# Performance work log

Hardware: AMD Instinct MI355X
Metric: run time of the kernel (lower is better)

Reference implementation:

```python
import jax, jax.numpy as jnp
import numpy as np

NUM_HEADS = 8
D_MODEL = 256
D_K = 256
SEQ = 32
FFT_HEAD = 3  # heads >= 3 operate in the FFT domain and are IFFT'd after
NEG = jnp.float32(1e10)


def _fft_t(x):
    # x: (..., 32, 256) real. Interleaved real/imag pairs -> complex 2D FFT over (4,2).
    lead = x.shape[:-2]
    xr = x.reshape(lead + (16, 32, 4, 2, 2))
    xc = jax.lax.complex(xr[..., 0], xr[..., 1])      # (..., 16, 32, 4, 2)
    y = jnp.fft.fft2(xc)                              # over last two axes
    out = jnp.concatenate([jnp.real(y), jnp.imag(y)], axis=-1)  # (...,16,32,4,4)
    return out.reshape(lead + (SEQ, D_MODEL))


def _ifft_t(x):
    lead = x.shape[:-2]
    xr = x.reshape(lead + (16, 32, 4, 2, 2))
    xc = jax.lax.complex(xr[..., 0], xr[..., 1])
    y = jnp.fft.ifft2(xc)
    out = jnp.concatenate([jnp.real(y), jnp.imag(y)], axis=-1)
    return out.reshape(lead + (SEQ, D_MODEL))


def _atrous_mask():
    i = jnp.arange(SEQ)[:, None]
    j = jnp.arange(SEQ)[None, :]
    return (jnp.abs(i - j) % 2 == 0).astype(jnp.float32)  # (32, 32)


def _attn_group(x, Wq_g, Wk_g, Wv_g, mask):
    # x: (B, S, D); W*_g: (H, D, K); mask: (S, S)
    Q = jnp.einsum('bsd,hdk->bhsk', x, Wq_g)
    K = jnp.einsum('bsd,hdk->bhsk', x, Wk_g)
    V = jnp.einsum('bsd,hdk->bhsk', x, Wv_g)
    scores = jnp.einsum('bhsk,bhtk->bhst', Q, K) / jnp.sqrt(jnp.float32(D_K))
    scores = scores * mask - NEG * (1.0 - mask)
    A = jax.nn.softmax(scores, axis=-1)
    return jnp.einsum('bhst,bhtk->bhsk', A, V)  # (B, H, S, K)


def setup_inputs() -> dict:
    key = jax.random.key(0)
    k0, k1, k2, k3 = jax.random.split(key, 4)
    B = 4096
    glorot = float(np.sqrt(2.0 / (D_MODEL + D_K)))
    return {
        'inputs': jax.random.normal(k0, (B, 1, SEQ, D_MODEL), dtype=jnp.float32),
        'Wq': jax.random.normal(k1, (NUM_HEADS, D_MODEL, D_K), dtype=jnp.float32) * glorot,
        'Wk': jax.random.normal(k2, (NUM_HEADS, D_MODEL, D_K), dtype=jnp.float32) * glorot,
        'Wv': jax.random.normal(k3, (NUM_HEADS, D_MODEL, D_K), dtype=jnp.float32) * glorot,
    }


def reference(inputs, Wq, Wk, Wv):
    # inputs: (B, 1, 32, 256)
    x = inputs[:, 0]                                  # (B, 32, 256)
    mask = _atrous_mask()
    # Heads 0..2: plain domain
    out_lo = _attn_group(x, Wq[:FFT_HEAD], Wk[:FFT_HEAD], Wv[:FFT_HEAD], mask)
    # Heads 3..: FFT domain, outputs IFFT'd per head
    xf = _fft_t(x)
    out_hi = _attn_group(xf, Wq[FFT_HEAD:], Wk[FFT_HEAD:], Wv[FFT_HEAD:], mask)
    out_hi = _ifft_t(out_hi)
    total = out_lo.sum(axis=1) + out_hi.sum(axis=1)   # (B, 32, 256)
    return (total / NUM_HEADS)[:, None]               # (B, 1, 32, 256)
```

## Files before the change

### kernel.cpp

```cpp
#include <hip/hip_runtime.h>

typedef _Float16 f16;
typedef _Float16 f16x4 __attribute__((ext_vector_type(4)));
typedef _Float16 f16x8 __attribute__((ext_vector_type(8)));
typedef float    f32x4 __attribute__((ext_vector_type(4)));

#define MFMA_F16(a,b,c) __builtin_amdgcn_mfma_f32_16x16x32_f16((a),(b),(c),0,0,0)

__device__ __forceinline__ float T_val(int rr, int cc) {
  int p = rr >> 2, f = rr & 3;
  int c = cc >> 2, d = (cc >> 1) & 1, e = cc & 1;
  int q = f & 1;
  int m = (p * c + 2 * q * d) & 3;
  float cs = (m == 0) ? 1.f : (m == 2) ? -1.f : 0.f;
  float sn = (m == 1) ? 1.f : (m == 3) ? -1.f : 0.f;
  if (f < 2) return (e == 0) ? cs : sn;
  return (e == 0) ? -sn : cs;
}
__device__ __forceinline__ float U_val(int rr, int cc) {
  int p = rr >> 2, f = rr & 3;
  int c = cc >> 2, d = (cc >> 1) & 1, e = cc & 1;
  int q = f & 1;
  int m = (p * c + 2 * q * d) & 3;
  float cs = (m == 0) ? 1.f : (m == 2) ? -1.f : 0.f;
  float sn = (m == 1) ? 1.f : (m == 3) ? -1.f : 0.f;
  float v;
  if (f < 2) v = (e == 0) ? cs : -sn;
  else       v = (e == 0) ? sn : cs;
  return v * 0.125f;
}

__global__ void prep_qk(const float* __restrict__ Wq, const float* __restrict__ Wk,
                        float* __restrict__ WqE, float* __restrict__ WkE) {
  int b = blockIdx.x;
  int isK = b >> 11;
  int h = (b >> 8) & 7;
  int dd = b & 255;
  const float* W = isK ? Wk : Wq;
  float* E = isK ? WkE : WqE;
  int k = threadIdx.x;
  size_t base = (size_t)h * 65536;
  float v;
  if (h < 3) {
    v = W[base + (size_t)dd * 256 + k];
  } else {
    int g = dd >> 4, i = dd & 15;
    float s = 0.f;
    for (int ip = 0; ip < 16; ++ip) {
      float t = T_val(ip, i);
      if (t != 0.f) s += t * W[base + (size_t)(g * 16 + ip) * 256 + k];
    }
    v = s;
  }
  E[base + (size_t)dd * 256 + k] = v;
}

__global__ void prep_m(const float* __restrict__ WqE, const float* __restrict__ WkE,
                       f16* __restrict__ Mt) {
  __shared__ float Aq[32][33];
  __shared__ float Bk[32][33];
  int h = blockIdx.x >> 6;
  int dpt = (blockIdx.x >> 3) & 7;
  int dt = blockIdx.x & 7;
  int tid = threadIdx.x;
  int drow = tid & 31;
  int dprow4 = (tid >> 5) * 4;
  float acc0 = 0.f, acc1 = 0.f, acc2 = 0.f, acc3 = 0.f;
  int r = tid >> 3;
  int c0 = (tid & 7) * 4;
  for (int kt = 0; kt < 8; ++kt) {
    for (int j = 0; j < 4; ++j) {
      Aq[r][c0 + j] = WqE[(size_t)h * 65536 + (size_t)(dt * 32 + r) * 256 + kt * 32 + c0 + j];
      Bk[r][c0 + j] = WkE[(size_t)h * 65536 + (size_t)(dpt * 32 + r) * 256 + kt * 32 + c0 + j];
    }
    __syncthreads();
    #pragma unroll
    for (int k = 0; k < 32; ++k) {
      float a = Aq[drow][k];
      acc0 += a * Bk[dprow4 + 0][k];
      acc1 += a * Bk[dprow4 + 1][k];
      acc2 += a * Bk[dprow4 + 2][k];
      acc3 += a * Bk[dprow4 + 3][k];
    }
    __syncthreads();
  }
  int d_ = dt * 32 + drow;
  size_t ob = (size_t)h * 65536 + (size_t)(dpt * 32 + dprow4) * 256 + d_;
  Mt[ob + 0 * 256] = (f16)(acc0 * 0.0625f);
  Mt[ob + 1 * 256] = (f16)(acc1 * 0.0625f);
  Mt[ob + 2 * 256] = (f16)(acc2 * 0.0625f);
  Mt[ob + 3 * 256] = (f16)(acc3 * 0.0625f);
}

__global__ void prep_v(const float* __restrict__ Wv, f16* __restrict__ Wvt) {
  __shared__ float Ts[16][16];
  __shared__ float Us[16][16];
  int h = blockIdx.x >> 8;
  int kp = blockIdx.x & 255;
  int tid = threadIdx.x;
  Ts[tid >> 4][tid & 15] = T_val(tid >> 4, tid & 15);
  Us[tid >> 4][tid & 15] = U_val(tid >> 4, tid & 15);
  __syncthreads();
  int d = tid;
  int g = d >> 4, i = d & 15;
  int gp = kp >> 4, fp = kp & 15;
  float s = 0.f;
  if (h < 3) {
    s = Wv[(size_t)h * 65536 + (size_t)d * 256 + kp];
  } else {
    for (int ip = 0; ip < 16; ++ip) {
      float tv = Ts[ip][i];
      if (tv != 0.f) {
        float inner = 0.f;
        for (int j = 0; j < 16; ++j) {
          float uv = Us[fp][j];
          if (uv != 0.f)
            inner += uv * Wv[(size_t)h * 65536 + (size_t)(g * 16 + ip) * 256 + gp * 16 + j];
        }
        s += tv * inner;
      }
    }
  }
  Wvt[(size_t)h * 65536 + (size_t)kp * 256 + d] = (f16)(s * 0.125f);
}

__device__ __forceinline__ int swz(int row, int col) { return col ^ ((row & 7) << 3); }

__global__ __launch_bounds__(512, 2) void mha_main(
    const float* __restrict__ xg_all,
    const f16* __restrict__ MtG,
    const f16* __restrict__ WvtG,
    float* __restrict__ outG)
{
  extern __shared__ char smem[];
  f16* Xs  = (f16*)smem;
  f16* Y   = (f16*)(smem + 65536);
  f16* VT  = (f16*)(smem + 65536);
  f16* Aat = (f16*)(smem + 135168);

  const int tid = threadIdx.x;
  const int w   = tid >> 6;
  const int l   = tid & 63;
  const int l15 = l & 15;
  const int l4  = l >> 4;

  f32x4 acc[8][2];
  #pragma unroll
  for (int i = 0; i < 8; ++i) {
    acc[i][0] = (f32x4){0.f, 0.f, 0.f, 0.f};
    acc[i][1] = (f32x4){0.f, 0.f, 0.f, 0.f};
  }

  const float* xg = xg_all + (size_t)blockIdx.x * 32768;
  #pragma unroll
  for (int i = 0; i < 16; ++i) {
    int f4 = i * 512 + tid;
    int row = f4 >> 6;
    int col = (f4 & 63) << 2;
    f32x4 v = *(const f32x4*)(xg + (size_t)f4 * 4);
    f16x4 hv = __builtin_convertvector(v, f16x4);
    *(f16x4*)(Xs + row * 256 + swz(row, col)) = hv;
  }
  __syncthreads();

  for (int h = 0; h < 8; ++h) {
    const f16* MtH = MtG + (size_t)h * 65536;
    const f16* WvH = WvtG + (size_t)h * 65536;

    f32x4 C0[8], C1[8];
    #pragma unroll
    for (int nt = 0; nt < 8; ++nt) {
      C0[nt] = (f32x4){0.f, 0.f, 0.f, 0.f};
      C1[nt] = (f32x4){0.f, 0.f, 0.f, 0.f};
    }
    {
      int arow = w * 32 + l15;
      #pragma unroll
      for (int kt = 0; kt < 8; ++kt) {
        int ks = kt * 32 + l4 * 8;
        f16x8 a0 = *(const f16x8*)(MtH + (size_t)arow * 256 + ks);
        f16x8 a1 = *(const f16x8*)(MtH + (size_t)(arow + 16) * 256 + ks);
        #pragma unroll
        for (int nt = 0; nt < 8; ++nt) {
          int xrow = nt * 16 + l15;
          f16x8 b = *(const f16x8*)(Xs + xrow * 256 + swz(xrow, ks));
          C0[nt] = MFMA_F16(a0, b, C0[nt]);
          C1[nt] = MFMA_F16(a1, b, C1[nt]);
        }
      }
      #pragma unroll
      for (int nt = 0; nt < 8; ++nt) {
        int srow = nt * 16 + l15;
        int dc0 = w * 32 + l4 * 4;
        *(f16x4*)(Y + srow * 256 + swz(srow, dc0)) = __builtin_convertvector(C0[nt], f16x4);
        *(f16x4*)(Y + srow * 256 + swz(srow, dc0 + 16)) = __builtin_convertvector(C1[nt], f16x4);
      }
    }
    __syncthreads();

    {
      int bq = w >> 1, mt = w & 1;
      f32x4 S0 = (f32x4){0.f, 0.f, 0.f, 0.f};
      f32x4 S1 = (f32x4){0.f, 0.f, 0.f, 0.f};
      int yrow = bq * 32 + mt * 16 + l15;
      int x0 = bq * 32 + l15;
      int x1 = bq * 32 + 16 + l15;
      #pragma unroll
      for (int kt = 0; kt < 8; ++kt) {
        int ks = kt * 32 + l4 * 8;
        f16x8 ay = *(const f16x8*)(Y + yrow * 256 + swz(yrow, ks));
        f16x8 b0 = *(const f16x8*)(Xs + x0 * 256 + swz(x0, ks));
        f16x8 b1 = *(const f16x8*)(Xs + x1 * 256 + swz(x1, ks));
        S0 = MFMA_F16(ay, b0, S0);
        S1 = MFMA_F16(ay, b1, S1);
      }
      #pragma unroll
      for (int r = 0; r < 4; ++r) {
        bool valid = ((l & 1) == (r & 1));
        float v0 = valid ? S0[r] : -1e30f;
        float v1 = valid ? S1[r] : -1e30f;
        float mx = fmaxf(v0, v1);
        mx = fmaxf(mx, __shfl_xor(mx, 1));
        mx = fmaxf(mx, __shfl_xor(mx, 2));
        mx = fmaxf(mx, __shfl_xor(mx, 4));
        mx = fmaxf(mx, __shfl_xor(mx, 8));
        float e0 = valid ? __expf(v0 - mx) : 0.f;
        float e1 = valid ? __expf(v1 - mx) : 0.f;
        float sm = e0 + e1;
        sm += __shfl_xor(sm, 1);
        sm += __shfl_xor(sm, 2);
        sm += __shfl_xor(sm, 4);
        sm += __shfl_xor(sm, 8);
        float inv = 1.f / sm;
        int s = mt * 16 + l4 * 4 + r;
        Aat[(bq * 32 + s) * 40 + l15] = (f16)(e0 * inv);
        Aat[(bq * 32 + s) * 40 + 16 + l15] = (f16)(e1 * inv);
      }
    }
    __syncthreads();

    f32x4 Cv0[8], Cv1[8];
    #pragma unroll
    for (int mt = 0; mt < 8; ++mt) {
      Cv0[mt] = (f32x4){0.f, 0.f, 0.f, 0.f};
      Cv1[mt] = (f32x4){0.f, 0.f, 0.f, 0.f};
    }
    {
      int bcol = w * 32 + l15;
      #pragma unroll
      for (int kt = 0; kt < 8; ++kt) {
        int ks = kt * 32 + l4 * 8;
        f16x8 b0 = *(const f16x8*)(WvH + (size_t)bcol * 256 + ks);
        f16x8 b1 = *(const f16x8*)(WvH + (size_t)(bcol + 16) * 256 + ks);
        #pragma unroll
        for (int mt = 0; mt < 8; ++mt) {
          int xrow = mt * 16 + l15;
          f16x8 a = *(const f16x8*)(Xs + xrow * 256 + swz(xrow, ks));
          Cv0[mt] = MFMA_F16(a, b0, Cv0[mt]);
          Cv1[mt] = MFMA_F16(a, b1, Cv1[mt]);
        }
      }
      #pragma unroll
      for (int mt = 0; mt < 8; ++mt) {
        int sp = mt * 16 + l4 * 4;
        int kp0 = w * 32 + l15;
        *(f16x4*)(VT + kp0 * 136 + sp) = __builtin_convertvector(Cv0[mt], f16x4);
        *(f16x4*)(VT + (kp0 + 16) * 136 + sp) = __builtin_convertvector(Cv1[mt], f16x4);
      }
    }
    __syncthreads();

    {
      int bo = w >> 1, kh = w & 1;
      f16x8 bf0 = *(const f16x8*)(Aat + (bo * 32 + l15) * 40 + l4 * 8);
      f16x8 bf1 = *(const f16x8*)(Aat + (bo * 32 + 16 + l15) * 40 + l4 * 8);
      #pragma unroll
      for (int mt = 0; mt < 8; ++mt) {
        int kp = kh * 128 + mt * 16 + l15;
        f16x8 av = *(const f16x8*)(VT + kp * 136 + bo * 32 + l4 * 8);
        acc[mt][0] = MFMA_F16(av, bf0, acc[mt][0]);
        acc[mt][1] = MFMA_F16(av, bf1, acc[mt][1]);
      }
    }
    __syncthreads();
  }

  {
    int bo = w >> 1, kh = w & 1;
    float* outB = outG + ((size_t)blockIdx.x * 4 + bo) * 8192;
    #pragma unroll
    for (int mt = 0; mt < 8; ++mt) {
      #pragma unroll
      for (int nt = 0; nt < 2; ++nt) {
        int s = nt * 16 + l15;
        int kp = kh * 128 + mt * 16 + l4 * 4;
        *(f32x4*)(outB + s * 256 + kp) = acc[mt][nt];
      }
    }
  }
}

extern "C" void kernel_launch(void* const* d_in, const int* in_sizes, int n_in,
                              void* d_out, int out_size, void* d_ws, size_t ws_size,
                              hipStream_t stream) {
  const float* x  = (const float*)d_in[0];
  const float* Wq = (const float*)d_in[1];
  const float* Wk = (const float*)d_in[2];
  const float* Wv = (const float*)d_in[3];
  float* out = (float*)d_out;
  char* ws = (char*)d_ws;
  float* WqE = (float*)ws;
  float* WkE = (float*)(ws + 2097152);
  f16*   Mt  = (f16*)(ws + 4194304);
  f16*   Wvt = (f16*)(ws + 5242880);

  prep_qk<<<4096, 256, 0, stream>>>(Wq, Wk, WqE, WkE);
  prep_m<<<512, 256, 0, stream>>>(WqE, WkE, Mt);
  prep_v<<<2048, 256, 0, stream>>>(Wv, Wvt);
  mha_main<<<1024, 512, 145408, stream>>>(x, Mt, Wvt, out);
}
```

Baseline: 437.3 us.

## Restructure attention kernel around 32x32 MFMA with register-resident intermediates

The main kernel now handles 8 batch elements per block (half as many blocks) and switches from 16x16x32 to 32x32x16 MFMAs. Each wave processes two batches and one head per pass. The Y (x·M) and V projections stay in registers and feed the score and output MFMAs directly, so the Y and V^T round-trips through LDS go away. Only the softmax probabilities go through shared memory, with two syncs per head pair instead of four per head. The costs are heavier register pressure, larger LDS use per block, and fewer blocks to fill the GPU.

Result: slower. 724.0 us (+65.6%).

```diff
diff --git a/kernel.cpp b/kernel.cpp
--- a/kernel.cpp
+++ b/kernel.cpp
@@ -4,8 +4,9 @@
 typedef _Float16 f16x4 __attribute__((ext_vector_type(4)));
 typedef _Float16 f16x8 __attribute__((ext_vector_type(8)));
 typedef float    f32x4 __attribute__((ext_vector_type(4)));
-
-#define MFMA_F16(a,b,c) __builtin_amdgcn_mfma_f32_16x16x32_f16((a),(b),(c),0,0,0)
+typedef float    f32x16 __attribute__((ext_vector_type(16)));
+
+#define MFMA32(a,b,c) __builtin_amdgcn_mfma_f32_32x32x16_f16((a),(b),(c),0,0,0)
 
 __device__ __forceinline__ float T_val(int rr, int cc) {
   int p = rr >> 2, f = rr & 3;
@@ -69,9 +70,9 @@
   int r = tid >> 3;
   int c0 = (tid & 7) * 4;
   for (int kt = 0; kt < 8; ++kt) {
-    for (int j = 0; j < 4; ++j) {
-      Aq[r][c0 + j] = WqE[(size_t)h * 65536 + (size_t)(dt * 32 + r) * 256 + kt * 32 + c0 + j];
-      Bk[r][c0 + j] = WkE[(size_t)h * 65536 + (size_t)(dpt * 32 + r) * 256 + kt * 32 + c0 + j];
+    for (int jj = 0; jj < 4; ++jj) {
+      Aq[r][c0 + jj] = WqE[(size_t)h * 65536 + (size_t)(dt * 32 + r) * 256 + kt * 32 + c0 + jj];
+      Bk[r][c0 + jj] = WkE[(size_t)h * 65536 + (size_t)(dpt * 32 + r) * 256 + kt * 32 + c0 + jj];
     }
     __syncthreads();
     #pragma unroll
@@ -112,10 +113,10 @@
       float tv = Ts[ip][i];
       if (tv != 0.f) {
         float inner = 0.f;
-        for (int j = 0; j < 16; ++j) {
-          float uv = Us[fp][j];
+        for (int jj = 0; jj < 16; ++jj) {
+          float uv = Us[fp][jj];
           if (uv != 0.f)
-            inner += uv * Wv[(size_t)h * 65536 + (size_t)(g * 16 + ip) * 256 + gp * 16 + j];
+            inner += uv * Wv[(size_t)h * 65536 + (size_t)(g * 16 + ip) * 256 + gp * 16 + jj];
         }
         s += tv * inner;
       }
@@ -124,7 +125,51 @@
   Wvt[(size_t)h * 65536 + (size_t)kp * 256 + d] = (f16)(s * 0.125f);
 }
 
-__device__ __forceinline__ int swz(int row, int col) { return col ^ ((row & 7) << 3); }
+__device__ __forceinline__ f16x8 cvt_lo(const f32x16& c) {
+  f16x8 r;
+  #pragma unroll
+  for (int i = 0; i < 8; ++i) r[i] = (f16)c[i];
+  return r;
+}
+__device__ __forceinline__ f16x8 cvt_hi(const f32x16& c) {
+  f16x8 r;
+  #pragma unroll
+  for (int i = 0; i < 8; ++i) r[i] = (f16)c[8 + i];
+  return r;
+}
+__device__ __forceinline__ f16x8 comb(f16x4 a, f16x4 b) {
+  f16x8 r;
+  #pragma unroll
+  for (int i = 0; i < 4; ++i) { r[i] = a[i]; r[4 + i] = b[i]; }
+  return r;
+}
+
+__device__ __forceinline__ void softmax_store(const f32x16& S, f16* Pb, int s, int H) {
+  int s1 = s & 1;
+  float mx = -1e30f;
+  #pragma unroll
+  for (int rr = 0; rr < 16; ++rr) {
+    float v = ((rr & 1) == s1) ? S[rr] : -1e30f;
+    mx = fmaxf(mx, v);
+  }
+  mx = fmaxf(mx, __shfl_xor(mx, 32));
+  float e[16];
+  float sum = 0.f;
+  #pragma unroll
+  for (int rr = 0; rr < 16; ++rr) {
+    float v = ((rr & 1) == s1) ? __expf(S[rr] - mx) : 0.f;
+    e[rr] = v;
+    sum += v;
+  }
+  sum += __shfl_xor(sum, 32);
+  float inv = 1.f / sum;
+  int px = (s & 7) << 2;
+  #pragma unroll
+  for (int rr = 0; rr < 16; ++rr) {
+    int t = (rr & 3) + 8 * (rr >> 2) + 4 * H;
+    Pb[s * 32 + (t ^ px)] = (f16)(e[rr] * inv);
+  }
+}
 
 __global__ __launch_bounds__(512, 2) void mha_main(
     const float* __restrict__ xg_all,
@@ -133,168 +178,130 @@
     float* __restrict__ outG)
 {
   extern __shared__ char smem[];
-  f16* Xs  = (f16*)smem;
-  f16* Y   = (f16*)(smem + 65536);
-  f16* VT  = (f16*)(smem + 65536);
-  f16* Aat = (f16*)(smem + 135168);
+  f16* Xs = (f16*)smem;
+  f16* Pl = (f16*)(smem + 131072);
 
   const int tid = threadIdx.x;
   const int w   = tid >> 6;
-  const int l   = tid & 63;
-  const int l15 = l & 15;
-  const int l4  = l >> 4;
-
-  f32x4 acc[8][2];
-  #pragma unroll
-  for (int i = 0; i < 8; ++i) {
-    acc[i][0] = (f32x4){0.f, 0.f, 0.f, 0.f};
-    acc[i][1] = (f32x4){0.f, 0.f, 0.f, 0.f};
-  }
-
-  const float* xg = xg_all + (size_t)blockIdx.x * 32768;
-  #pragma unroll
-  for (int i = 0; i < 16; ++i) {
+  const int l31 = tid & 31;
+  const int H   = (tid >> 5) & 1;
+  const int bp  = w >> 1;
+  const int j   = w & 1;
+
+  const float* xg = xg_all + (size_t)blockIdx.x * 65536;
+  #pragma unroll 4
+  for (int i = 0; i < 32; ++i) {
     int f4 = i * 512 + tid;
     int row = f4 >> 6;
-    int col = (f4 & 63) << 2;
+    int col4 = (f4 & 63) << 2;
     f32x4 v = *(const f32x4*)(xg + (size_t)f4 * 4);
-    f16x4 hv = __builtin_convertvector(v, f16x4);
-    *(f16x4*)(Xs + row * 256 + swz(row, col)) = hv;
+    f16x4 hv;
+    hv[0] = (f16)v[0]; hv[1] = (f16)v[1]; hv[2] = (f16)v[2]; hv[3] = (f16)v[3];
+    *(f16x4*)(Xs + row * 256 + (col4 ^ ((row & 7) << 3))) = hv;
   }
   __syncthreads();
 
-  for (int h = 0; h < 8; ++h) {
-    const f16* MtH = MtG + (size_t)h * 65536;
-    const f16* WvH = WvtG + (size_t)h * 65536;
-
-    f32x4 C0[8], C1[8];
+  const int b0 = bp * 2, b1 = b0 + 1;
+  const f16* Xr0 = Xs + (b0 * 32 + l31) * 256;
+  const f16* Xr1 = Xs + (b1 * 32 + l31) * 256;
+  const int rx = (l31 & 7) << 3;
+
+  f32x16 acc[2][4];
+  #pragma unroll
+  for (int bb = 0; bb < 2; ++bb)
     #pragma unroll
-    for (int nt = 0; nt < 8; ++nt) {
-      C0[nt] = (f32x4){0.f, 0.f, 0.f, 0.f};
-      C1[nt] = (f32x4){0.f, 0.f, 0.f, 0.f};
-    }
+    for (int t4 = 0; t4 < 4; ++t4)
+      #pragma unroll
+      for (int i = 0; i < 16; ++i) acc[bb][t4][i] = 0.f;
+
+  for (int r = 0; r < 4; ++r) {
     {
-      int arow = w * 32 + l15;
+      const f16* MtH = MtG + (size_t)(2 * r + j) * 65536;
+      f32x16 S0, S1;
       #pragma unroll
-      for (int kt = 0; kt < 8; ++kt) {
-        int ks = kt * 32 + l4 * 8;
-        f16x8 a0 = *(const f16x8*)(MtH + (size_t)arow * 256 + ks);
-        f16x8 a1 = *(const f16x8*)(MtH + (size_t)(arow + 16) * 256 + ks);
+      for (int i = 0; i < 16; ++i) { S0[i] = 0.f; S1[i] = 0.f; }
+      for (int dt = 0; dt < 8; ++dt) {
+        f32x16 Y0, Y1;
         #pragma unroll
-        for (int nt = 0; nt < 8; ++nt) {
-          int xrow = nt * 16 + l15;
-          f16x8 b = *(const f16x8*)(Xs + xrow * 256 + swz(xrow, ks));
-          C0[nt] = MFMA_F16(a0, b, C0[nt]);
-          C1[nt] = MFMA_F16(a1, b, C1[nt]);
+        for (int i = 0; i < 16; ++i) { Y0[i] = 0.f; Y1[i] = 0.f; }
+        const f16* Arow = MtH + (size_t)(dt * 32 + l31) * 256 + H * 8;
+        #pragma unroll 4
+        for (int kt = 0; kt < 16; ++kt) {
+          f16x8 a = *(const f16x8*)(Arow + kt * 16);
+          int sc = (kt * 16 + H * 8) ^ rx;
+          f16x8 xb0 = *(const f16x8*)(Xr0 + sc);
+          f16x8 xb1 = *(const f16x8*)(Xr1 + sc);
+          Y0 = MFMA32(a, xb0, Y0);
+          Y1 = MFMA32(a, xb1, Y1);
         }
+        int c0 = (dt * 32 + 4 * H) ^ rx;
+        int c1 = (dt * 32 + 4 * H + 8) ^ rx;
+        int c2 = (dt * 32 + 16 + 4 * H) ^ rx;
+        int c3 = (dt * 32 + 24 + 4 * H) ^ rx;
+        f16x8 alo0 = comb(*(const f16x4*)(Xr0 + c0), *(const f16x4*)(Xr0 + c1));
+        f16x8 ahi0 = comb(*(const f16x4*)(Xr0 + c2), *(const f16x4*)(Xr0 + c3));
+        f16x8 alo1 = comb(*(const f16x4*)(Xr1 + c0), *(const f16x4*)(Xr1 + c1));
+        f16x8 ahi1 = comb(*(const f16x4*)(Xr1 + c2), *(const f16x4*)(Xr1 + c3));
+        S0 = MFMA32(alo0, cvt_lo(Y0), S0);
+        S0 = MFMA32(ahi0, cvt_hi(Y0), S0);
+        S1 = MFMA32(alo1, cvt_lo(Y1), S1);
+        S1 = MFMA32(ahi1, cvt_hi(Y1), S1);
       }
+      softmax_store(S0, Pl + (j * 8 + b0) * 1024, l31, H);
+      softmax_store(S1, Pl + (j * 8 + b1) * 1024, l31, H);
+    }
+    __syncthreads();
+    #pragma unroll
+    for (int hh = 0; hh < 2; ++hh) {
+      const f16* WvH = WvtG + (size_t)(2 * r + hh) * 65536;
+      const f16* Pb0 = Pl + (hh * 8 + b0) * 1024 + l31 * 32;
+      const f16* Pb1 = Pl + (hh * 8 + b1) * 1024 + l31 * 32;
+      int px = (l31 & 7) << 2;
+      f16x8 P0lo = comb(*(const f16x4*)(Pb0 + ((4 * H) ^ px)),
+                        *(const f16x4*)(Pb0 + ((4 * H + 8) ^ px)));
+      f16x8 P0hi = comb(*(const f16x4*)(Pb0 + ((16 + 4 * H) ^ px)),
+                        *(const f16x4*)(Pb0 + ((24 + 4 * H) ^ px)));
+      f16x8 P1lo = comb(*(const f16x4*)(Pb1 + ((4 * H) ^ px)),
+                        *(const f16x4*)(Pb1 + ((4 * H + 8) ^ px)));
+      f16x8 P1hi = comb(*(const f16x4*)(Pb1 + ((16 + 4 * H) ^ px)),
+                        *(const f16x4*)(Pb1 + ((24 + 4 * H) ^ px)));
       #pragma unroll
-      for (int nt = 0; nt < 8; ++nt) {
-        int srow = nt * 16 + l15;
-        int dc0 = w * 32 + l4 * 4;
-        *(f16x4*)(Y + srow * 256 + swz(srow, dc0)) = __builtin_convertvector(C0[nt], f16x4);
-        *(f16x4*)(Y + srow * 256 + swz(srow, dc0 + 16)) = __builtin_convertvector(C1[nt], f16x4);
+      for (int t4 = 0; t4 < 4; ++t4) {
+        const f16* Wrow = WvH + (size_t)((j * 4 + t4) * 32 + l31) * 256 + H * 8;
+        f32x16 V0, V1;
+        #pragma unroll
+        for (int i = 0; i < 16; ++i) { V0[i] = 0.f; V1[i] = 0.f; }
+        #pragma unroll 4
+        for (int kt = 0; kt < 16; ++kt) {
+          f16x8 wv = *(const f16x8*)(Wrow + kt * 16);
+          int sc = (kt * 16 + H * 8) ^ rx;
+          f16x8 xa0 = *(const f16x8*)(Xr0 + sc);
+          f16x8 xa1 = *(const f16x8*)(Xr1 + sc);
+          V0 = MFMA32(xa0, wv, V0);
+          V1 = MFMA32(xa1, wv, V1);
+        }
+        acc[0][t4] = MFMA32(cvt_lo(V0), P0lo, acc[0][t4]);
+        acc[0][t4] = MFMA32(cvt_hi(V0), P0hi, acc[0][t4]);
+        acc[1][t4] = MFMA32(cvt_lo(V1), P1lo, acc[1][t4]);
+        acc[1][t4] = MFMA32(cvt_hi(V1), P1hi, acc[1][t4]);
       }
     }
     __syncthreads();
-
-    {
-      int bq = w >> 1, mt = w & 1;
-      f32x4 S0 = (f32x4){0.f, 0.f, 0.f, 0.f};
-      f32x4 S1 = (f32x4){0.f, 0.f, 0.f, 0.f};
-      int yrow = bq * 32 + mt * 16 + l15;
-      int x0 = bq * 32 + l15;
-      int x1 = bq * 32 + 16 + l15;
+  }
+
+  #pragma unroll
+  for (int bb = 0; bb < 2; ++bb) {
+    float* ob = outG + ((size_t)blockIdx.x * 8 + (bp * 2 + bb)) * 8192 + l31 * 256 + j * 128;
+    #pragma unroll
+    for (int t4 = 0; t4 < 4; ++t4) {
       #pragma unroll
-      for (int kt = 0; kt < 8; ++kt) {
-        int ks = kt * 32 + l4 * 8;
-        f16x8 ay = *(const f16x8*)(Y + yrow * 256 + swz(yrow, ks));
-        f16x8 b0 = *(const f16x8*)(Xs + x0 * 256 + swz(x0, ks));
-        f16x8 b1 = *(const f16x8*)(Xs + x1 * 256 + swz(x1, ks));
-        S0 = MFMA_F16(ay, b0, S0);
-        S1 = MFMA_F16(ay, b1, S1);
-      }
-      #pragma unroll
-      for (int r = 0; r < 4; ++r) {
-        bool valid = ((l & 1) == (r & 1));
-        float v0 = valid ? S0[r] : -1e30f;
-        float v1 = valid ? S1[r] : -1e30f;
-        float mx = fmaxf(v0, v1);
-        mx = fmaxf(mx, __shfl_xor(mx, 1));
-        mx = fmaxf(mx, __shfl_xor(mx, 2));
-        mx = fmaxf(mx, __shfl_xor(mx, 4));
-        mx = fmaxf(mx, __shfl_xor(mx, 8));
-        float e0 = valid ? __expf(v0 - mx) : 0.f;
-        float e1 = valid ? __expf(v1 - mx) : 0.f;
-        float sm = e0 + e1;
-        sm += __shfl_xor(sm, 1);
-        sm += __shfl_xor(sm, 2);
-        sm += __shfl_xor(sm, 4);
-        sm += __shfl_xor(sm, 8);
-        float inv = 1.f / sm;
-        int s = mt * 16 + l4 * 4 + r;
-        Aat[(bq * 32 + s) * 40 + l15] = (f16)(e0 * inv);
-        Aat[(bq * 32 + s) * 40 + 16 + l15] = (f16)(e1 * inv);
-      }
-    }
-    __syncthreads();
-
-    f32x4 Cv0[8], Cv1[8];
-    #pragma unroll
-    for (int mt = 0; mt < 8; ++mt) {
-      Cv0[mt] = (f32x4){0.f, 0.f, 0.f, 0.f};
-      Cv1[mt] = (f32x4){0.f, 0.f, 0.f, 0.f};
-    }
-    {
-      int bcol = w * 32 + l15;
-      #pragma unroll
-      for (int kt = 0; kt < 8; ++kt) {
-        int ks = kt * 32 + l4 * 8;
-        f16x8 b0 = *(const f16x8*)(WvH + (size_t)bcol * 256 + ks);
-        f16x8 b1 = *(const f16x8*)(WvH + (size_t)(bcol + 16) * 256 + ks);
-        #pragma unroll
-        for (int mt = 0; mt < 8; ++mt) {
-          int xrow = mt * 16 + l15;
-          f16x8 a = *(const f16x8*)(Xs + xrow * 256 + swz(xrow, ks));
-          Cv0[mt] = MFMA_F16(a, b0, Cv0[mt]);
-          Cv1[mt] = MFMA_F16(a, b1, Cv1[mt]);
-        }
-      }
-      #pragma unroll
-      for (int mt = 0; mt < 8; ++mt) {
-        int sp = mt * 16 + l4 * 4;
-        int kp0 = w * 32 + l15;
-        *(f16x4*)(VT + kp0 * 136 + sp) = __builtin_convertvector(Cv0[mt], f16x4);
-        *(f16x4*)(VT + (kp0 + 16) * 136 + sp) = __builtin_convertvector(Cv1[mt], f16x4);
-      }
-    }
-    __syncthreads();
-
-    {
-      int bo = w >> 1, kh = w & 1;
-      f16x8 bf0 = *(const f16x8*)(Aat + (bo * 32 + l15) * 40 + l4 * 8);
-      f16x8 bf1 = *(const f16x8*)(Aat + (bo * 32 + 16 + l15) * 40 + l4 * 8);
-      #pragma unroll
-      for (int mt = 0; mt < 8; ++mt) {
-        int kp = kh * 128 + mt * 16 + l15;
-        f16x8 av = *(const f16x8*)(VT + kp * 136 + bo * 32 + l4 * 8);
-        acc[mt][0] = MFMA_F16(av, bf0, acc[mt][0]);
-        acc[mt][1] = MFMA_F16(av, bf1, acc[mt][1]);
-      }
-    }
-    __syncthreads();
-  }
-
-  {
-    int bo = w >> 1, kh = w & 1;
-    float* outB = outG + ((size_t)blockIdx.x * 4 + bo) * 8192;
-    #pragma unroll
-    for (int mt = 0; mt < 8; ++mt) {
-      #pragma unroll
-      for (int nt = 0; nt < 2; ++nt) {
-        int s = nt * 16 + l15;
-        int kp = kh * 128 + mt * 16 + l4 * 4;
-        *(f32x4*)(outB + s * 256 + kp) = acc[mt][nt];
+      for (int q = 0; q < 4; ++q) {
+        f32x4 v;
+        v[0] = acc[bb][t4][q * 4 + 0];
+        v[1] = acc[bb][t4][q * 4 + 1];
+        v[2] = acc[bb][t4][q * 4 + 2];
+        v[3] = acc[bb][t4][q * 4 + 3];
+        *(f32x4*)(ob + t4 * 32 + q * 8 + H * 4) = v;
       }
     }
   }
@@ -317,5 +324,5 @@
   prep_qk<<<4096, 256, 0, stream>>>(Wq, Wk, WqE, WkE);
   prep_m<<<512, 256, 0, stream>>>(WqE, WkE, Mt);
   prep_v<<<2048, 256, 0, stream>>>(Wv, Wvt);
-  mha_main<<<1024, 512, 145408, stream>>>(x, Mt, Wvt, out);
-}
+  mha_main<<<512, 512, 163840, stream>>>(x, Mt, Wvt, out);
+}
```

## Keep V in registers, retile per-head GEMMs, and pre-pack weights into MFMA fragment layout

Applied to the files above, without the earlier changes.

Weights Mt and Wvt are repacked by a new small kernel into a layout ordered by MFMA fragment, so each lane loads its operand with one coalesced 16-byte read. The per-head Q·M and X·Wv GEMMs are retiled into 4x4 and 2x2x4 register blocks per wave, which raises operand reuse. The V projection result now stays in registers as packed f16 and feeds the A·V MFMA directly. This removes the VT shared-memory staging and one barrier per head, in exchange for higher register pressure and an extra launch.

New measurement: 430.6 us. Within noise of the previous version (-1.5%).

```diff
diff --git a/kernel.cpp b/kernel.cpp
--- a/kernel.cpp
+++ b/kernel.cpp
@@ -4,8 +4,21 @@
 typedef _Float16 f16x4 __attribute__((ext_vector_type(4)));
 typedef _Float16 f16x8 __attribute__((ext_vector_type(8)));
 typedef float    f32x4 __attribute__((ext_vector_type(4)));
+typedef unsigned int u32;
 
 #define MFMA_F16(a,b,c) __builtin_amdgcn_mfma_f32_16x16x32_f16((a),(b),(c),0,0,0)
+
+__device__ __forceinline__ u32 pkf16(float a, float b) {
+  return __builtin_bit_cast(u32, __builtin_amdgcn_cvt_pkrtz(a, b));
+}
+union F8U4 { u32 d[4]; f16x8 v; };
+
+__device__ __forceinline__ f16x8 comb(f16x4 a, f16x4 b) {
+  f16x8 r;
+  #pragma unroll
+  for (int i = 0; i < 4; ++i) { r[i] = a[i]; r[4 + i] = b[i]; }
+  return r;
+}
 
 __device__ __forceinline__ float T_val(int rr, int cc) {
   int p = rr >> 2, f = rr & 3;
@@ -69,9 +82,9 @@
   int r = tid >> 3;
   int c0 = (tid & 7) * 4;
   for (int kt = 0; kt < 8; ++kt) {
-    for (int j = 0; j < 4; ++j) {
-      Aq[r][c0 + j] = WqE[(size_t)h * 65536 + (size_t)(dt * 32 + r) * 256 + kt * 32 + c0 + j];
-      Bk[r][c0 + j] = WkE[(size_t)h * 65536 + (size_t)(dpt * 32 + r) * 256 + kt * 32 + c0 + j];
+    for (int jj = 0; jj < 4; ++jj) {
+      Aq[r][c0 + jj] = WqE[(size_t)h * 65536 + (size_t)(dt * 32 + r) * 256 + kt * 32 + c0 + jj];
+      Bk[r][c0 + jj] = WkE[(size_t)h * 65536 + (size_t)(dpt * 32 + r) * 256 + kt * 32 + c0 + jj];
     }
     __syncthreads();
     #pragma unroll
@@ -112,10 +125,10 @@
       float tv = Ts[ip][i];
       if (tv != 0.f) {
         float inner = 0.f;
-        for (int j = 0; j < 16; ++j) {
-          float uv = Us[fp][j];
+        for (int jj = 0; jj < 16; ++jj) {
+          float uv = Us[fp][jj];
           if (uv != 0.f)
-            inner += uv * Wv[(size_t)h * 65536 + (size_t)(g * 16 + ip) * 256 + gp * 16 + j];
+            inner += uv * Wv[(size_t)h * 65536 + (size_t)(g * 16 + ip) * 256 + gp * 16 + jj];
         }
         s += tv * inner;
       }
@@ -124,19 +137,31 @@
   Wvt[(size_t)h * 65536 + (size_t)kp * 256 + d] = (f16)(s * 0.125f);
 }
 
-__device__ __forceinline__ int swz(int row, int col) { return col ^ ((row & 7) << 3); }
+__global__ void repack16(const f16* __restrict__ Mt, const f16* __restrict__ Wvt,
+                         f16* __restrict__ MtF, f16* __restrict__ WvF) {
+  int bid = blockIdx.x;
+  int which = bid >> 10;
+  int h = (bid >> 7) & 7;
+  int t16 = (bid >> 3) & 15;
+  int kt = bid & 7;
+  int l = threadIdx.x;
+  const f16* src = which ? Wvt : Mt;
+  f16* dst = which ? WvF : MtF;
+  size_t sb = (size_t)h * 65536 + (size_t)(t16 * 16 + (l & 15)) * 256 + kt * 32 + (l >> 4) * 8;
+  size_t db = ((size_t)((h * 16 + t16) * 8 + kt) * 64 + l) * 8;
+  *(f16x8*)(dst + db) = *(const f16x8*)(src + sb);
+}
 
 __global__ __launch_bounds__(512, 2) void mha_main(
     const float* __restrict__ xg_all,
-    const f16* __restrict__ MtG,
-    const f16* __restrict__ WvtG,
+    const f16* __restrict__ MtF,
+    const f16* __restrict__ WvF,
     float* __restrict__ outG)
 {
   extern __shared__ char smem[];
   f16* Xs  = (f16*)smem;
   f16* Y   = (f16*)(smem + 65536);
-  f16* VT  = (f16*)(smem + 65536);
-  f16* Aat = (f16*)(smem + 135168);
+  f16* Aat = (f16*)(smem + 131072);
 
   const int tid = threadIdx.x;
   const int w   = tid >> 6;
@@ -144,62 +169,111 @@
   const int l15 = l & 15;
   const int l4  = l >> 4;
 
-  f32x4 acc[8][2];
-  #pragma unroll
-  for (int i = 0; i < 8; ++i) {
-    acc[i][0] = (f32x4){0.f, 0.f, 0.f, 0.f};
-    acc[i][1] = (f32x4){0.f, 0.f, 0.f, 0.f};
-  }
-
   const float* xg = xg_all + (size_t)blockIdx.x * 32768;
-  #pragma unroll
+  #pragma unroll 4
   for (int i = 0; i < 16; ++i) {
     int f4 = i * 512 + tid;
     int row = f4 >> 6;
     int col = (f4 & 63) << 2;
     f32x4 v = *(const f32x4*)(xg + (size_t)f4 * 4);
-    f16x4 hv = __builtin_convertvector(v, f16x4);
-    *(f16x4*)(Xs + row * 256 + swz(row, col)) = hv;
+    f16x4 hv;
+    hv[0] = (f16)v[0]; hv[1] = (f16)v[1]; hv[2] = (f16)v[2]; hv[3] = (f16)v[3];
+    *(f16x4*)(Xs + row * 256 + (col ^ ((row & 7) << 3))) = hv;
   }
   __syncthreads();
 
+  const int dq = w >> 1, sh = w & 1;
+  const int bp = w >> 2, kq = w & 3;
+  const int bq = w >> 1, mt = w & 1;
+
+  f32x4 O[2][2][4];
+  #pragma unroll
+  for (int b = 0; b < 2; ++b)
+    #pragma unroll
+    for (int sm = 0; sm < 2; ++sm)
+      #pragma unroll
+      for (int n = 0; n < 4; ++n)
+        O[b][sm][n] = (f32x4){0.f, 0.f, 0.f, 0.f};
+
   for (int h = 0; h < 8; ++h) {
-    const f16* MtH = MtG + (size_t)h * 65536;
-    const f16* WvH = WvtG + (size_t)h * 65536;
-
-    f32x4 C0[8], C1[8];
-    #pragma unroll
-    for (int nt = 0; nt < 8; ++nt) {
-      C0[nt] = (f32x4){0.f, 0.f, 0.f, 0.f};
-      C1[nt] = (f32x4){0.f, 0.f, 0.f, 0.f};
-    }
     {
-      int arow = w * 32 + l15;
-      #pragma unroll
+      f32x4 C[4][4];
+      #pragma unroll
+      for (int a = 0; a < 4; ++a)
+        #pragma unroll
+        for (int n = 0; n < 4; ++n) C[a][n] = (f32x4){0.f, 0.f, 0.f, 0.f};
+      #pragma unroll 2
       for (int kt = 0; kt < 8; ++kt) {
-        int ks = kt * 32 + l4 * 8;
-        f16x8 a0 = *(const f16x8*)(MtH + (size_t)arow * 256 + ks);
-        f16x8 a1 = *(const f16x8*)(MtH + (size_t)(arow + 16) * 256 + ks);
-        #pragma unroll
-        for (int nt = 0; nt < 8; ++nt) {
-          int xrow = nt * 16 + l15;
-          f16x8 b = *(const f16x8*)(Xs + xrow * 256 + swz(xrow, ks));
-          C0[nt] = MFMA_F16(a0, b, C0[nt]);
-          C1[nt] = MFMA_F16(a1, b, C1[nt]);
+        f16x8 A[4], B[4];
+        #pragma unroll
+        for (int a = 0; a < 4; ++a)
+          A[a] = *(const f16x8*)(MtF + ((size_t)((h * 16 + dq * 4 + a) * 8 + kt) * 64 + l) * 8);
+        #pragma unroll
+        for (int n = 0; n < 4; ++n) {
+          int srow = sh * 64 + n * 16 + l15;
+          B[n] = *(const f16x8*)(Xs + srow * 256 + ((kt * 32 + l4 * 8) ^ ((srow & 7) << 3)));
         }
-      }
-      #pragma unroll
-      for (int nt = 0; nt < 8; ++nt) {
-        int srow = nt * 16 + l15;
-        int dc0 = w * 32 + l4 * 4;
-        *(f16x4*)(Y + srow * 256 + swz(srow, dc0)) = __builtin_convertvector(C0[nt], f16x4);
-        *(f16x4*)(Y + srow * 256 + swz(srow, dc0 + 16)) = __builtin_convertvector(C1[nt], f16x4);
-      }
+        #pragma unroll
+        for (int a = 0; a < 4; ++a)
+          #pragma unroll
+          for (int n = 0; n < 4; ++n)
+            C[a][n] = MFMA_F16(A[a], B[n], C[a][n]);
+      }
+      #pragma unroll
+      for (int a = 0; a < 4; ++a)
+        #pragma unroll
+        for (int n = 0; n < 4; ++n) {
+          int srow = sh * 64 + n * 16 + l15;
+          int dcol = dq * 64 + a * 16 + l4 * 4;
+          f16x4 hv;
+          hv[0] = (f16)C[a][n][0]; hv[1] = (f16)C[a][n][1];
+          hv[2] = (f16)C[a][n][2]; hv[3] = (f16)C[a][n][3];
+          *(f16x4*)(Y + srow * 256 + (dcol ^ ((srow & 7) << 3))) = hv;
+        }
+    }
+    u32 Vh[2][2][4][2];
+    {
+      f32x4 VC[2][2][4];
+      #pragma unroll
+      for (int b = 0; b < 2; ++b)
+        #pragma unroll
+        for (int tau = 0; tau < 2; ++tau)
+          #pragma unroll
+          for (int n = 0; n < 4; ++n) VC[b][tau][n] = (f32x4){0.f, 0.f, 0.f, 0.f};
+      #pragma unroll 2
+      for (int kt = 0; kt < 8; ++kt) {
+        f16x8 Bw[4], Ax[2][2];
+        #pragma unroll
+        for (int n = 0; n < 4; ++n)
+          Bw[n] = *(const f16x8*)(WvF + ((size_t)((h * 16 + kq * 4 + n) * 8 + kt) * 64 + l) * 8);
+        #pragma unroll
+        for (int b = 0; b < 2; ++b)
+          #pragma unroll
+          for (int tau = 0; tau < 2; ++tau) {
+            int xrow = (bp * 2 + b) * 32 + tau * 16 + l15;
+            Ax[b][tau] = *(const f16x8*)(Xs + xrow * 256 + ((kt * 32 + l4 * 8) ^ ((xrow & 7) << 3)));
+          }
+        #pragma unroll
+        for (int b = 0; b < 2; ++b)
+          #pragma unroll
+          for (int tau = 0; tau < 2; ++tau)
+            #pragma unroll
+            for (int n = 0; n < 4; ++n)
+              VC[b][tau][n] = MFMA_F16(Ax[b][tau], Bw[n], VC[b][tau][n]);
+      }
+      #pragma unroll
+      for (int b = 0; b < 2; ++b)
+        #pragma unroll
+        for (int tau = 0; tau < 2; ++tau)
+          #pragma unroll
+          for (int n = 0; n < 4; ++n) {
+            Vh[b][tau][n][0] = pkf16(VC[b][tau][n][0], VC[b][tau][n][1]);
+            Vh[b][tau][n][1] = pkf16(VC[b][tau][n][2], VC[b][tau][n][3]);
+          }
     }
     __syncthreads();
 
     {
-      int bq = w >> 1, mt = w & 1;
       f32x4 S0 = (f32x4){0.f, 0.f, 0.f, 0.f};
       f32x4 S1 = (f32x4){0.f, 0.f, 0.f, 0.f};
       int yrow = bq * 32 + mt * 16 + l15;
@@ -208,9 +282,9 @@
       #pragma unroll
       for (int kt = 0; kt < 8; ++kt) {
         int ks = kt * 32 + l4 * 8;
-        f16x8 ay = *(const f16x8*)(Y + yrow * 256 + swz(yrow, ks));
-        f16x8 b0 = *(const f16x8*)(Xs + x0 * 256 + swz(x0, ks));
-        f16x8 b1 = *(const f16x8*)(Xs + x1 * 256 + swz(x1, ks));
+        f16x8 ay = *(const f16x8*)(Y + yrow * 256 + (ks ^ ((yrow & 7) << 3)));
+        f16x8 b0 = *(const f16x8*)(Xs + x0 * 256 + (ks ^ ((x0 & 7) << 3)));
+        f16x8 b1 = *(const f16x8*)(Xs + x1 * 256 + (ks ^ ((x1 & 7) << 3)));
         S0 = MFMA_F16(ay, b0, S0);
         S1 = MFMA_F16(ay, b1, S1);
       }
@@ -239,62 +313,36 @@
     }
     __syncthreads();
 
-    f32x4 Cv0[8], Cv1[8];
     #pragma unroll
-    for (int mt = 0; mt < 8; ++mt) {
-      Cv0[mt] = (f32x4){0.f, 0.f, 0.f, 0.f};
-      Cv1[mt] = (f32x4){0.f, 0.f, 0.f, 0.f};
-    }
-    {
-      int bcol = w * 32 + l15;
-      #pragma unroll
-      for (int kt = 0; kt < 8; ++kt) {
-        int ks = kt * 32 + l4 * 8;
-        f16x8 b0 = *(const f16x8*)(WvH + (size_t)bcol * 256 + ks);
-        f16x8 b1 = *(const f16x8*)(WvH + (size_t)(bcol + 16) * 256 + ks);
-        #pragma unroll
-        for (int mt = 0; mt < 8; ++mt) {
-          int xrow = mt * 16 + l15;
-          f16x8 a = *(const f16x8*)(Xs + xrow * 256 + swz(xrow, ks));
-          Cv0[mt] = MFMA_F16(a, b0, Cv0[mt]);
-          Cv1[mt] = MFMA_F16(a, b1, Cv1[mt]);
+    for (int b = 0; b < 2; ++b) {
+      #pragma unroll
+      for (int sm = 0; sm < 2; ++sm) {
+        int arow = ((bp * 2 + b) * 32 + sm * 16 + l15) * 40 + l4 * 4;
+        f16x8 bf = comb(*(const f16x4*)(Aat + arow),
+                        *(const f16x4*)(Aat + arow + 16));
+        #pragma unroll
+        for (int n = 0; n < 4; ++n) {
+          F8U4 av;
+          av.d[0] = Vh[b][0][n][0];
+          av.d[1] = Vh[b][0][n][1];
+          av.d[2] = Vh[b][1][n][0];
+          av.d[3] = Vh[b][1][n][1];
+          O[b][sm][n] = MFMA_F16(av.v, bf, O[b][sm][n]);
         }
       }
-      #pragma unroll
-      for (int mt = 0; mt < 8; ++mt) {
-        int sp = mt * 16 + l4 * 4;
-        int kp0 = w * 32 + l15;
-        *(f16x4*)(VT + kp0 * 136 + sp) = __builtin_convertvector(Cv0[mt], f16x4);
-        *(f16x4*)(VT + (kp0 + 16) * 136 + sp) = __builtin_convertvector(Cv1[mt], f16x4);
-      }
-    }
-    __syncthreads();
-
-    {
-      int bo = w >> 1, kh = w & 1;
-      f16x8 bf0 = *(const f16x8*)(Aat + (bo * 32 + l15) * 40 + l4 * 8);
-      f16x8 bf1 = *(const f16x8*)(Aat + (bo * 32 + 16 + l15) * 40 + l4 * 8);
-      #pragma unroll
-      for (int mt = 0; mt < 8; ++mt) {
-        int kp = kh * 128 + mt * 16 + l15;
-        f16x8 av = *(const f16x8*)(VT + kp * 136 + bo * 32 + l4 * 8);
-        acc[mt][0] = MFMA_F16(av, bf0, acc[mt][0]);
-        acc[mt][1] = MFMA_F16(av, bf1, acc[mt][1]);
-      }
-    }
-    __syncthreads();
-  }
-
-  {
-    int bo = w >> 1, kh = w & 1;
-    float* outB = outG + ((size_t)blockIdx.x * 4 + bo) * 8192;
+    }
+  }
+
+  #pragma unroll
+  for (int b = 0; b < 2; ++b) {
+    float* ob = outG + ((size_t)blockIdx.x * 4 + bp * 2 + b) * 8192;
     #pragma unroll
-    for (int mt = 0; mt < 8; ++mt) {
-      #pragma unroll
-      for (int nt = 0; nt < 2; ++nt) {
-        int s = nt * 16 + l15;
-        int kp = kh * 128 + mt * 16 + l4 * 4;
-        *(f32x4*)(outB + s * 256 + kp) = acc[mt][nt];
+    for (int sm = 0; sm < 2; ++sm) {
+      int s = sm * 16 + l15;
+      #pragma unroll
+      for (int n = 0; n < 4; ++n) {
+        int kp = kq * 64 + n * 16 + l4 * 4;
+        *(f32x4*)(ob + s * 256 + kp) = O[b][sm][n];
       }
     }
   }
@@ -313,9 +361,12 @@
   float* WkE = (float*)(ws + 2097152);
   f16*   Mt  = (f16*)(ws + 4194304);
   f16*   Wvt = (f16*)(ws + 5242880);
+  f16*   MtF = (f16*)ws;
+  f16*   WvF = (f16*)(ws + 2097152);
 
   prep_qk<<<4096, 256, 0, stream>>>(Wq, Wk, WqE, WkE);
   prep_m<<<512, 256, 0, stream>>>(WqE, WkE, Mt);
   prep_v<<<2048, 256, 0, stream>>>(Wv, Wvt);
-  mha_main<<<1024, 512, 145408, stream>>>(x, Mt, Wvt, out);
-}
+  repack16<<<2048, 64, 0, stream>>>(Mt, Wvt, MtF, WvF);
+  mha_main<<<1024, 512, 141312, stream>>>(x, MtF, WvF, out);
+}
```
